# Optimization experiments

Hardware: AMD Instinct MI355X
Metric: run time of the kernel (lower is better)

## Reference

```python
import jax, jax.numpy as jnp
import numpy as np

LOG2E = 1.4426950408889634  # 1/ln(2): convert natural-log gates to log2 space (kernel uses exp2)
BT = 64  # chunk size


def setup_inputs() -> dict:
    key = jax.random.key(0)
    ks = jax.random.split(key, 5)
    B, H, T, K, V = 4, 8, 4096, 128, 128
    return {
        "q": jax.random.normal(ks[0], (B, H, T, K), dtype=jnp.float32),
        "k": jax.random.normal(ks[1], (B, H, T, K), dtype=jnp.float32),
        "v": jax.random.normal(ks[2], (B, H, T, V), dtype=jnp.float32),
        "i_gate": jax.random.normal(ks[3], (B, H, T), dtype=jnp.float32),
        "f_gate": jax.random.normal(ks[4], (B, H, T), dtype=jnp.float32),
    }


def reference(q, k, v, i_gate, f_gate):
    B, H, T, K = q.shape
    V = v.shape[-1]
    NT = T // BT
    scale = K ** -0.5

    # gate preprocessing: log-sigmoid forget gate, both gates moved to log2 space
    vecF = jax.nn.log_sigmoid(f_gate) * LOG2E  # [B,H,T]
    vecI = i_gate * LOG2E                      # [B,H,T]

    f_c = vecF.reshape(B, H, NT, BT)
    i_c = vecI.reshape(B, H, NT, BT)
    qc = q.reshape(B, H, NT, BT, K)
    kc = k.reshape(B, H, NT, BT, K)
    vc = v.reshape(B, H, NT, BT, V)

    vecB = jnp.cumsum(f_c, axis=-1)            # inclusive cumsum of f within chunk [B,H,NT,BT]
    scaG = vecB[..., -1]                       # total decay per chunk [B,H,NT]
    vecA = i_c + (scaG[..., None] - vecB)      # i_j + sum of f after j within chunk

    # ---- inter-chunk recurrence over matrix state C, normalizer n, max m ----
    kx = jnp.moveaxis(kc, 2, 0)  # [NT,B,H,BT,K]
    vx = jnp.moveaxis(vc, 2, 0)
    ax = jnp.moveaxis(vecA, 2, 0)  # [NT,B,H,BT]
    gx = jnp.moveaxis(scaG, 2, 0)  # [NT,B,H]

    C0 = jnp.zeros((B, H, K, V), dtype=q.dtype)
    n0 = jnp.zeros((B, H, K), dtype=q.dtype)
    m0 = jnp.zeros((B, H), dtype=q.dtype)

    def step(carry, inp):
        C, n, m = carry
        kk, vv, a, g = inp
        m_next = jnp.maximum(g + m, jnp.max(a, axis=-1))      # running stabilizer max
        dec = jnp.exp2(g + m - m_next)                        # [B,H]
        kbar = kk * jnp.exp2(a - m_next[..., None])[..., None]
        C_next = C * dec[..., None, None] + jnp.einsum('bhtk,bhtv->bhkv', kbar, vv)
        n_next = n * dec[..., None] + kbar.sum(axis=-2)
        return (C_next, n_next, m_next), (C, n, m)

    _, (Cp, np_, mp) = jax.lax.scan(step, (C0, n0, m0), (kx, vx, ax, gx))
    Cp = jnp.moveaxis(Cp, 0, 2)   # state entering each chunk [B,H,NT,K,V]
    np_ = jnp.moveaxis(np_, 0, 2)  # [B,H,NT,K]
    mp = jnp.moveaxis(mp, 0, 2)   # [B,H,NT]

    # ---- intra-chunk parallel part ----
    idx = jnp.arange(BT)
    causal = idx[:, None] >= idx[None, :]  # query i attends key j<=i
    # logD[i,j] = B_i - B_j + I_j for j<=i
    logD = vecB[..., :, None] - vecB[..., None, :] + i_c[..., None, :]
    logD = jnp.where(causal, logD, -jnp.inf)
    m_intra = logD.max(axis=-1)                                   # [B,H,NT,BT]
    m_comb = jnp.maximum(mp[..., None] + vecB, m_intra)           # total stabilizer per row
    D = jnp.exp2(logD - m_comb[..., None])                        # masked entries -> 0

    S = jnp.einsum('bhcik,bhcjk->bhcij', qc, kc) * scale * D
    qbar = qc * (scale * jnp.exp2(vecB + mp[..., None] - m_comb))[..., None]

    Hnum = jnp.einsum('bhcik,bhckv->bhciv', qbar, Cp) + jnp.einsum('bhcij,bhcjv->bhciv', S, vc)
    den = jnp.einsum('bhcik,bhck->bhci', qbar, np_) + S.sum(axis=-1)
    norm = jnp.maximum(jnp.abs(den), jnp.exp2(-m_comb))
    h = Hnum / norm[..., None]
    return h.reshape(B, H, T, V)
```

## Files before the change

### kernel.cpp

```cpp
#include <hip/hip_runtime.h>
#include <hip/hip_bf16.h>
#include <math.h>


#define LOG2E 1.4426950408889634f
constexpr int Bsz = 4, Hsz = 8, Tsz = 4096, Ksz = 128, Vsz = 128;
constexpr int BT = 64, NT = 64, BH = Bsz * Hsz;
constexpr float SCALE = 0.08838834764831845f;

typedef __attribute__((ext_vector_type(8))) short short8v;
typedef __attribute__((ext_vector_type(4))) float f32x4;
typedef __attribute__((ext_vector_type(4))) unsigned short u16x4;
typedef __attribute__((ext_vector_type(8))) unsigned short u16x8;

__device__ inline float bf2f(unsigned short u) {
    union { unsigned int i; float f; } c; c.i = ((unsigned int)u) << 16; return c.f;
}
__device__ inline unsigned short f2bf(float f) {
    __hip_bfloat16 h = __float2bfloat16(f);
    union { __hip_bfloat16 b; unsigned short u; } cv; cv.b = h; return cv.u;
}

__global__ __launch_bounds__(64) void k_gates(
    const float* __restrict__ ig, const float* __restrict__ fg,
    float* __restrict__ vecB, float* __restrict__ vecI, float* __restrict__ vecA,
    float* __restrict__ mintra, float* __restrict__ scaG, float* __restrict__ scaA)
{
    int c = blockIdx.x, bh = blockIdx.y, lane = threadIdx.x;
    int t = bh * Tsz + c * BT + lane;
    float f = fg[t];
    float ls = fminf(f, 0.f) - log1pf(expf(-fabsf(f)));
    float vF = ls * LOG2E;
    float vI = ig[t] * LOG2E;
    float b = vF;
    #pragma unroll
    for (int off = 1; off < 64; off <<= 1) {
        float o = __shfl_up(b, off, 64);
        if (lane >= off) b += o;
    }
    float g = __shfl(b, 63, 64);
    float mi = vI - b;
    #pragma unroll
    for (int off = 1; off < 64; off <<= 1) {
        float o = __shfl_up(mi, off, 64);
        if (lane >= off) mi = fmaxf(mi, o);
    }
    float a = vI + g - b;
    vecB[t] = b; vecI[t] = vI; vecA[t] = a; mintra[t] = b + mi;
    float am = a;
    #pragma unroll
    for (int off = 32; off; off >>= 1) am = fmaxf(am, __shfl_xor(am, off, 64));
    if (lane == 0) { scaG[bh * NT + c] = g; scaA[bh * NT + c] = am; }
}

__global__ __launch_bounds__(64) void k_mscan(
    const float* __restrict__ scaG, const float* __restrict__ scaA,
    float* __restrict__ mp, float* __restrict__ dec)
{
    int bh = blockIdx.x, lane = threadIdx.x;
    float g0 = scaG[bh * NT + lane];
    float a = g0, b = scaA[bh * NT + lane];
    #pragma unroll
    for (int off = 1; off < 64; off <<= 1) {
        float ap = __shfl_up(a, off, 64);
        float bp = __shfl_up(b, off, 64);
        if (lane >= off) { b = fmaxf(bp + a, b); a = ap + a; }
    }
    float m_incl = fmaxf(a, b);
    float m_prev = __shfl_up(m_incl, 1, 64);
    if (lane == 0) { m_prev = 0.f; mp[bh * (NT + 1)] = 0.f; }
    mp[bh * (NT + 1) + lane + 1] = m_incl;
    dec[bh * NT + lane] = exp2f(g0 + m_prev - m_incl);
}

__global__ __launch_bounds__(256, 4) void k_state(
    const float* __restrict__ kg, const float* __restrict__ vg,
    const float* __restrict__ vecA, const float* __restrict__ mp,
    unsigned short* __restrict__ UT, float* __restrict__ nU)
{
    int c = blockIdx.x, bh = blockIdx.y, tid = threadIdx.x;
    int lane = tid & 63, wid = tid >> 6;
    int lrow = lane & 15, kgrp = lane >> 4;

    __shared__ __align__(16) unsigned short kThi[128][72];
    __shared__ __align__(16) unsigned short vTs[128][72];
    __shared__ float nUp[128][5];

    size_t hb = (size_t)bh * Tsz + (size_t)c * BT;
    float mpn = mp[bh * (NT + 1) + c + 1];

    int cb = tid & 15, jr = tid >> 4;
    int wboff = (((jr >> 1) ^ (cb & 7)) * 16) + (jr & 1) * 8;
    float s4[4];
    #pragma unroll
    for (int x = 0; x < 4; ++x) s4[x] = exp2f(vecA[hb + jr * 4 + x] - mpn);
    #pragma unroll
    for (int p = 0; p < 2; ++p) {
        int c0 = p * 64 + cb * 4;
        float ka[4][4], va[4][4];
        #pragma unroll
        for (int x = 0; x < 4; ++x) {
            float4 kr = *(const float4*)(kg + (hb + jr * 4 + x) * Ksz + c0);
            float4 vr = *(const float4*)(vg + (hb + jr * 4 + x) * Vsz + c0);
            ka[x][0] = kr.x; ka[x][1] = kr.y; ka[x][2] = kr.z; ka[x][3] = kr.w;
            va[x][0] = vr.x; va[x][1] = vr.y; va[x][2] = vr.z; va[x][3] = vr.w;
        }
        #pragma unroll
        for (int y = 0; y < 4; ++y) {
            u16x4 h, w;
            float psum = 0.f;
            #pragma unroll
            for (int x = 0; x < 4; ++x) {
                float f = ka[x][y] * s4[x];
                h[x] = f2bf(f);
                psum += f;
                w[x] = f2bf(va[x][y]);
            }
            *(u16x4*)((char*)&kThi[c0 + y][0] + wboff) = h;
            *(u16x4*)((char*)&vTs[c0 + y][0] + wboff) = w;
            psum += __shfl_xor(psum, 16, 64);
            psum += __shfl_xor(psum, 32, 64);
            if (kgrp == 0) nUp[c0 + y][wid] = psum;
        }
    }
    __syncthreads();

    f32x4 acc[2][8];
    #pragma unroll
    for (int kt = 0; kt < 2; ++kt)
        #pragma unroll
        for (int vt = 0; vt < 8; ++vt) acc[kt][vt] = (f32x4){0.f, 0.f, 0.f, 0.f};
    #pragma unroll
    for (int ks = 0; ks < 2; ++ks) {
        int G = ks * 4 + kgrp;
        #pragma unroll
        for (int kt = 0; kt < 2; ++kt) {
            int arow = (wid * 2 + kt) * 16 + lrow;
            short8v af = *(const short8v*)((const char*)&kThi[arow][0]
                                           + ((G ^ ((arow >> 2) & 7)) * 16));
            #pragma unroll
            for (int vt = 0; vt < 8; ++vt) {
                int brow = vt * 16 + lrow;
                short8v bv = *(const short8v*)((const char*)&vTs[brow][0]
                                               + ((G ^ ((brow >> 2) & 7)) * 16));
                acc[kt][vt] = __builtin_amdgcn_mfma_f32_16x16x32_bf16(af, bv, acc[kt][vt], 0, 0, 0);
            }
        }
    }
    unsigned short* Ub = UT + (size_t)(bh * NT + c) * (Ksz * Vsz);
    #pragma unroll
    for (int kt = 0; kt < 2; ++kt) {
        int ktile = wid * 2 + kt;
        #pragma unroll
        for (int vt = 0; vt < 8; ++vt) {
            u16x4 w;
            #pragma unroll
            for (int r = 0; r < 4; ++r) w[r] = f2bf(acc[kt][vt][r]);
            *(u16x4*)(Ub + ((size_t)(ktile * 8 + vt) * 64 + lane) * 4) = w;
        }
    }
    if (tid < Ksz) {
        float s = nUp[tid][0] + nUp[tid][1] + nUp[tid][2] + nUp[tid][3];
        nU[(size_t)(bh * NT + c) * Ksz + tid] = s;
    }
}

__global__ __launch_bounds__(128) void k_scan(
    unsigned short* __restrict__ UT, const float* __restrict__ dec,
    const float* __restrict__ nU, float* __restrict__ np)
{
    int s = blockIdx.x, bh = blockIdx.y, tid = threadIdx.x;
    __shared__ float decs[NT];
    if (tid < NT) decs[tid] = dec[bh * NT + tid];
    __syncthreads();
    if (s == 32) {
        float n = 0.f;
        size_t base = (size_t)bh * NT * Ksz + tid;
        #pragma unroll 4
        for (int c2 = 0; c2 < NT; ++c2) {
            float u = nU[base + (size_t)c2 * Ksz];
            np[base + (size_t)c2 * Ksz] = n;
            n = n * decs[c2] + u;
        }
        return;
    }
    size_t base = (size_t)bh * NT * (Ksz * Vsz) + s * 512 + tid * 4;
    float C0 = 0.f, C1 = 0.f, C2 = 0.f, C3 = 0.f;
    #pragma unroll 4
    for (int c2 = 0; c2 < NT; ++c2) {
        size_t idx = base + (size_t)c2 * (Ksz * Vsz);
        u16x4 u = *(const u16x4*)(UT + idx);
        u16x4 w;
        w.x = f2bf(C0); w.y = f2bf(C1); w.z = f2bf(C2); w.w = f2bf(C3);
        *(u16x4*)(UT + idx) = w;
        float d = decs[c2];
        C0 = C0 * d + bf2f(u.x); C1 = C1 * d + bf2f(u.y);
        C2 = C2 * d + bf2f(u.z); C3 = C3 * d + bf2f(u.w);
    }
}

__global__ __launch_bounds__(256, 4) void k_intra(
    const float* __restrict__ qg, const float* __restrict__ kgl, const float* __restrict__ vg,
    const float* __restrict__ vecB, const float* __restrict__ vecI,
    const float* __restrict__ mintra, const float* __restrict__ mp,
    const float* __restrict__ np, const unsigned short* __restrict__ CpT,
    float* __restrict__ out)
{
    int c = blockIdx.x, bh = blockIdx.y, tid = threadIdx.x;
    int lane = tid & 63, wid = tid >> 6;
    int lrow = lane & 15, kgrp = lane >> 4;

    __shared__ __align__(16) unsigned short R[17408];
    __shared__ float rowf[BT], colf[BT], sfqs[BT], emcs[BT], denb[BT], npv[Ksz];

    auto khi = (unsigned short(*)[136])R;
    auto klo = (unsigned short(*)[136])(R + 64 * 136);
    auto Sb  = (unsigned short(*)[72])R;
    unsigned short* vTf = R + 64 * 72;
    unsigned short* cpsF = R;

    size_t hb = (size_t)bh * Tsz + (size_t)c * BT;
    float mpc = mp[bh * (NT + 1) + c];
    if (tid < BT) {
        float b = vecB[hb + tid];
        float mc = fmaxf(mpc + b, mintra[hb + tid]);
        rowf[tid] = SCALE * exp2f(b - mc);
        colf[tid] = exp2f(vecI[hb + tid] - b);
        sfqs[tid] = SCALE * exp2f(b + mpc - mc);
        emcs[tid] = exp2f(-mc);
    }
    if (tid < Ksz) npv[tid] = np[((size_t)bh * NT + c) * Ksz + tid];

    const float4* k4 = (const float4*)(kgl + hb * Ksz);
    for (int e = tid; e < BT * Ksz / 4; e += 256) {
        int i = e >> 5, c4 = (e & 31) * 4;
        float4 kv = k4[e];
        u16x4 h, l;
        h.x = f2bf(kv.x); l.x = f2bf(kv.x - bf2f(h.x));
        h.y = f2bf(kv.y); l.y = f2bf(kv.y - bf2f(h.y));
        h.z = f2bf(kv.z); l.z = f2bf(kv.z - bf2f(h.z));
        h.w = f2bf(kv.w); l.w = f2bf(kv.w - bf2f(h.w));
        *(u16x4*)&khi[i][c4] = h; *(u16x4*)&klo[i][c4] = l;
    }
    const float* qrow = qg + (hb + wid * 16 + lrow) * Ksz;
    float qf[4][8];
    #pragma unroll
    for (int ks = 0; ks < 4; ++ks) {
        float4 a = *(const float4*)(qrow + ks * 32 + kgrp * 8);
        float4 b = *(const float4*)(qrow + ks * 32 + kgrp * 8 + 4);
        qf[ks][0] = a.x; qf[ks][1] = a.y; qf[ks][2] = a.z; qf[ks][3] = a.w;
        qf[ks][4] = b.x; qf[ks][5] = b.y; qf[ks][6] = b.z; qf[ks][7] = b.w;
    }
    int vcb = tid & 15, jb = tid >> 4;
    float vpre[2][4][4];
    #pragma unroll
    for (int p = 0; p < 2; ++p)
        #pragma unroll
        for (int x = 0; x < 4; ++x) {
            float4 r4 = *(const float4*)(vg + (hb + jb * 4 + x) * Vsz + p * 64 + vcb * 4);
            vpre[p][x][0] = r4.x; vpre[p][x][1] = r4.y; vpre[p][x][2] = r4.z; vpre[p][x][3] = r4.w;
        }
    __syncthreads();

    float dot = 0.f;
    #pragma unroll
    for (int ks = 0; ks < 4; ++ks)
        #pragma unroll
        for (int x = 0; x < 8; ++x) dot += qf[ks][x] * npv[ks * 32 + kgrp * 8 + x];
    dot += __shfl_xor(dot, 16, 64);
    dot += __shfl_xor(dot, 32, 64);
    float qdot = sfqs[wid * 16 + lrow] * dot;

    short8v qh[4], ql[4];
    #pragma unroll
    for (int ks = 0; ks < 4; ++ks)
        #pragma unroll
        for (int x = 0; x < 8; ++x) {
            float f = qf[ks][x];
            unsigned short hh = f2bf(f);
            qh[ks][x] = (short)hh;
            ql[ks][x] = (short)f2bf(f - bf2f(hh));
        }

    f32x4 accS[4];
    #pragma unroll
    for (int jt = 0; jt < 4; ++jt) accS[jt] = (f32x4){0.f, 0.f, 0.f, 0.f};
    #pragma unroll
    for (int ks = 0; ks < 4; ++ks) {
        #pragma unroll
        for (int jt = 0; jt < 4; ++jt) {
            if (jt <= wid) {
                short8v bh_ = *(const short8v*)&khi[jt * 16 + lrow][ks * 32 + kgrp * 8];
                short8v bl  = *(const short8v*)&klo[jt * 16 + lrow][ks * 32 + kgrp * 8];
                accS[jt] = __builtin_amdgcn_mfma_f32_16x16x32_bf16(qh[ks], bh_, accS[jt], 0, 0, 0);
                accS[jt] = __builtin_amdgcn_mfma_f32_16x16x32_bf16(ql[ks], bh_, accS[jt], 0, 0, 0);
                accS[jt] = __builtin_amdgcn_mfma_f32_16x16x32_bf16(qh[ks], bl,  accS[jt], 0, 0, 0);
            }
        }
    }

    float rsum[4] = {0.f, 0.f, 0.f, 0.f};
    unsigned short sreg[4][4];
    #pragma unroll
    for (int jt = 0; jt < 4; ++jt)
        #pragma unroll
        for (int r = 0; r < 4; ++r) {
            int i = wid * 16 + kgrp * 4 + r, j = jt * 16 + lrow;
            float val = (j <= i) ? accS[jt][r] * rowf[i] * colf[j] : 0.f;
            rsum[r] += val;
            sreg[jt][r] = f2bf(val);
        }
    #pragma unroll
    for (int r = 0; r < 4; ++r) {
        rsum[r] += __shfl_xor(rsum[r], 1, 64);
        rsum[r] += __shfl_xor(rsum[r], 2, 64);
        rsum[r] += __shfl_xor(rsum[r], 4, 64);
        rsum[r] += __shfl_xor(rsum[r], 8, 64);
    }
    float qd[4];
    #pragma unroll
    for (int r = 0; r < 4; ++r) qd[r] = __shfl(qdot, kgrp * 4 + r, 64);
    if (lrow == 0) {
        #pragma unroll
        for (int r = 0; r < 4; ++r) {
            int i = wid * 16 + kgrp * 4 + r;
            float den = qd[r] + rsum[r];
            denb[i] = 1.f / fmaxf(fabsf(den), emcs[i]);
        }
    }
    __syncthreads();

    const u16x8* Cg = (const u16x8*)(CpT + ((size_t)bh * NT + c) * (Ksz * Vsz));
    u16x8 cpre[8];
    #pragma unroll
    for (int p2 = 0; p2 < 8; ++p2) cpre[p2] = Cg[tid + p2 * 256];

    #pragma unroll
    for (int jt = 0; jt < 4; ++jt)
        #pragma unroll
        for (int r = 0; r < 4; ++r)
            Sb[wid * 16 + kgrp * 4 + r][jt * 16 + lrow] = sreg[jt][r];
    #pragma unroll
    for (int p = 0; p < 2; ++p)
        #pragma unroll
        for (int y = 0; y < 4; ++y) {
            int row = p * 64 + vcb * 4 + y;
            int swzb = (jb * 8) ^ ((row & 7) << 4);
            u16x4 w;
            #pragma unroll
            for (int x = 0; x < 4; ++x) w[x] = f2bf(vpre[p][x][y]);
            *(u16x4*)((char*)(vTf + row * 64) + swzb) = w;
        }
    __syncthreads();

    f32x4 accV[8];
    #pragma unroll
    for (int vt = 0; vt < 8; ++vt) accV[vt] = (f32x4){0.f, 0.f, 0.f, 0.f};
    #pragma unroll
    for (int ks = 0; ks < 2; ++ks) {
        short8v as_ = *(const short8v*)&Sb[wid * 16 + lrow][ks * 32 + kgrp * 8];
        #pragma unroll
        for (int vt = 0; vt < 8; ++vt) {
            int row = vt * 16 + lrow;
            int swzb = ((ks * 64 + kgrp * 16)) ^ ((row & 7) << 4);
            short8v bv = *(const short8v*)((const char*)(vTf + row * 64) + swzb);
            accV[vt] = __builtin_amdgcn_mfma_f32_16x16x32_bf16(as_, bv, accV[vt], 0, 0, 0);
        }
    }
    __syncthreads();

    #pragma unroll
    for (int p2 = 0; p2 < 8; ++p2) {
        int idx = tid + p2 * 256;
        *(u16x8*)&cpsF[idx * 8] = cpre[p2];
    }
    __syncthreads();

    f32x4 accC[8];
    #pragma unroll
    for (int vt = 0; vt < 8; ++vt) accC[vt] = (f32x4){0.f, 0.f, 0.f, 0.f};
    #pragma unroll
    for (int ks = 0; ks < 4; ++ks) {
        int ktile = ks * 2 + (kgrp >> 1);
        int lsrc = (kgrp & 1) * 32 + lrow;
        #pragma unroll
        for (int vt = 0; vt < 8; ++vt) {
            const unsigned short* pf = &cpsF[((ktile * 8 + vt) * 64 + lsrc) * 4];
            u16x4 lo4 = *(const u16x4*)pf;
            u16x4 hi4 = *(const u16x4*)(pf + 64);
            short8v bc;
            bc[0] = (short)lo4.x; bc[1] = (short)lo4.y; bc[2] = (short)lo4.z; bc[3] = (short)lo4.w;
            bc[4] = (short)hi4.x; bc[5] = (short)hi4.y; bc[6] = (short)hi4.z; bc[7] = (short)hi4.w;
            accC[vt] = __builtin_amdgcn_mfma_f32_16x16x32_bf16(qh[ks], bc, accC[vt], 0, 0, 0);
            accC[vt] = __builtin_amdgcn_mfma_f32_16x16x32_bf16(ql[ks], bc, accC[vt], 0, 0, 0);
        }
    }
    size_t gb = hb * Vsz;
    #pragma unroll
    for (int vt = 0; vt < 8; ++vt)
        #pragma unroll
        for (int r = 0; r < 4; ++r) {
            int i = wid * 16 + kgrp * 4 + r, vc = vt * 16 + lrow;
            out[gb + (size_t)i * Vsz + vc] = (sfqs[i] * accC[vt][r] + accV[vt][r]) * denb[i];
        }
}

extern "C" void kernel_launch(void* const* d_in, const int* in_sizes, int n_in,
                              void* d_out, int out_size, void* d_ws, size_t ws_size,
                              hipStream_t stream) {
    const float* q  = (const float*)d_in[0];
    const float* k  = (const float*)d_in[1];
    const float* v  = (const float*)d_in[2];
    const float* ig = (const float*)d_in[3];
    const float* fg = (const float*)d_in[4];
    float* out = (float*)d_out;

    float* ws = (float*)d_ws;
    float* vecB   = ws;
    float* vecI   = vecB + BH * Tsz;
    float* vecA   = vecI + BH * Tsz;
    float* mintra = vecA + BH * Tsz;
    float* scaG   = mintra + BH * Tsz;
    float* scaA   = scaG + BH * NT;
    float* dec    = scaA + BH * NT;
    float* mp     = dec + BH * NT;
    float* nU     = mp + BH * (NT + 1);
    float* np     = nU + BH * NT * Ksz;
    unsigned short* UT = (unsigned short*)(np + BH * NT * Ksz);

    k_gates<<<dim3(NT, BH), 64, 0, stream>>>(ig, fg, vecB, vecI, vecA, mintra, scaG, scaA);
    k_mscan<<<dim3(BH), 64, 0, stream>>>(scaG, scaA, mp, dec);
    k_state<<<dim3(NT, BH), 256, 0, stream>>>(k, v, vecA, mp, UT, nU);
    k_scan<<<dim3(33, BH), 128, 0, stream>>>(UT, dec, nU, np);
    k_intra<<<dim3(NT, BH), 256, 0, stream>>>(q, k, v, vecB, vecI, mintra, mp, np, UT, out);
}
```

Baseline: 119.7 us.

## Process four chunks per k_state block with double-buffered LDS and prefetch

k_state now handles CPB=4 chunks per block. It double-buffers the transposed k/v tiles in LDS and issues global loads for the next chunk into registers while the MFMA accumulation of the current chunk runs. The aim is to hide global load latency behind compute and to amortise block setup. The cost is more registers for the prefetch buffers, a launch bound lowered to 2 waves per SIMD, double the LDS, and a grid reduced to 512 blocks, which may lower occupancy and parallelism.

```diff
diff --git a/kernel.cpp b/kernel.cpp
--- a/kernel.cpp
+++ b/kernel.cpp
@@ -7,6 +7,7 @@
 constexpr int Bsz = 4, Hsz = 8, Tsz = 4096, Ksz = 128, Vsz = 128;
 constexpr int BT = 64, NT = 64, BH = Bsz * Hsz;
 constexpr float SCALE = 0.08838834764831845f;
+constexpr int CPB = 4;
 
 typedef __attribute__((ext_vector_type(8))) short short8v;
 typedef __attribute__((ext_vector_type(4))) float f32x4;
@@ -19,6 +20,9 @@
 __device__ inline unsigned short f2bf(float f) {
     __hip_bfloat16 h = __float2bfloat16(f);
     union { __hip_bfloat16 b; unsigned short u; } cv; cv.b = h; return cv.u;
+}
+__device__ inline float f4c(const float4& v, int y) {
+    return y == 0 ? v.x : y == 1 ? v.y : y == 2 ? v.z : v.w;
 }
 
 __global__ __launch_bounds__(64) void k_gates(
@@ -73,95 +77,116 @@
     dec[bh * NT + lane] = exp2f(g0 + m_prev - m_incl);
 }
 
-__global__ __launch_bounds__(256, 4) void k_state(
+__global__ __launch_bounds__(256, 2) void k_state(
     const float* __restrict__ kg, const float* __restrict__ vg,
     const float* __restrict__ vecA, const float* __restrict__ mp,
     unsigned short* __restrict__ UT, float* __restrict__ nU)
 {
-    int c = blockIdx.x, bh = blockIdx.y, tid = threadIdx.x;
+    int c0 = blockIdx.x * CPB, bh = blockIdx.y, tid = threadIdx.x;
     int lane = tid & 63, wid = tid >> 6;
     int lrow = lane & 15, kgrp = lane >> 4;
 
-    __shared__ __align__(16) unsigned short kThi[128][72];
-    __shared__ __align__(16) unsigned short vTs[128][72];
-    __shared__ float nUp[128][5];
-
-    size_t hb = (size_t)bh * Tsz + (size_t)c * BT;
-    float mpn = mp[bh * (NT + 1) + c + 1];
+    __shared__ __align__(16) unsigned short kT[2][128][72];
+    __shared__ __align__(16) unsigned short vT[2][128][72];
+    __shared__ float nUp[2][128][5];
 
     int cb = tid & 15, jr = tid >> 4;
     int wboff = (((jr >> 1) ^ (cb & 7)) * 16) + (jr & 1) * 8;
-    float s4[4];
-    #pragma unroll
-    for (int x = 0; x < 4; ++x) s4[x] = exp2f(vecA[hb + jr * 4 + x] - mpn);
-    #pragma unroll
-    for (int p = 0; p < 2; ++p) {
-        int c0 = p * 64 + cb * 4;
-        float ka[4][4], va[4][4];
-        #pragma unroll
-        for (int x = 0; x < 4; ++x) {
-            float4 kr = *(const float4*)(kg + (hb + jr * 4 + x) * Ksz + c0);
-            float4 vr = *(const float4*)(vg + (hb + jr * 4 + x) * Vsz + c0);
-            ka[x][0] = kr.x; ka[x][1] = kr.y; ka[x][2] = kr.z; ka[x][3] = kr.w;
-            va[x][0] = vr.x; va[x][1] = vr.y; va[x][2] = vr.z; va[x][3] = vr.w;
-        }
-        #pragma unroll
-        for (int y = 0; y < 4; ++y) {
-            u16x4 h, w;
-            float psum = 0.f;
-            #pragma unroll
-            for (int x = 0; x < 4; ++x) {
-                float f = ka[x][y] * s4[x];
-                h[x] = f2bf(f);
-                psum += f;
-                w[x] = f2bf(va[x][y]);
+    const float* mpb = mp + bh * (NT + 1);
+
+    float4 kreg[4][2], vreg[4][2];
+
+    auto issue_loads = [&](int cc) {
+        size_t hbc = (size_t)bh * Tsz + (size_t)(c0 + cc) * BT;
+        #pragma unroll
+        for (int x = 0; x < 4; ++x)
+            #pragma unroll
+            for (int p = 0; p < 2; ++p) {
+                kreg[x][p] = *(const float4*)(kg + (hbc + jr * 4 + x) * Ksz + p * 64 + cb * 4);
+                vreg[x][p] = *(const float4*)(vg + (hbc + jr * 4 + x) * Vsz + p * 64 + cb * 4);
             }
-            *(u16x4*)((char*)&kThi[c0 + y][0] + wboff) = h;
-            *(u16x4*)((char*)&vTs[c0 + y][0] + wboff) = w;
-            psum += __shfl_xor(psum, 16, 64);
-            psum += __shfl_xor(psum, 32, 64);
-            if (kgrp == 0) nUp[c0 + y][wid] = psum;
-        }
-    }
-    __syncthreads();
-
-    f32x4 acc[2][8];
-    #pragma unroll
-    for (int kt = 0; kt < 2; ++kt)
-        #pragma unroll
-        for (int vt = 0; vt < 8; ++vt) acc[kt][vt] = (f32x4){0.f, 0.f, 0.f, 0.f};
-    #pragma unroll
-    for (int ks = 0; ks < 2; ++ks) {
-        int G = ks * 4 + kgrp;
+    };
+    auto cvt_store = [&](int cc, int b) {
+        size_t hbc = (size_t)bh * Tsz + (size_t)(c0 + cc) * BT;
+        float mpn = mpb[c0 + cc + 1];
+        float s4[4];
+        #pragma unroll
+        for (int x = 0; x < 4; ++x) s4[x] = exp2f(vecA[hbc + jr * 4 + x] - mpn);
+        #pragma unroll
+        for (int p = 0; p < 2; ++p) {
+            int cb0 = p * 64 + cb * 4;
+            #pragma unroll
+            for (int y = 0; y < 4; ++y) {
+                u16x4 h, w;
+                float psum = 0.f;
+                #pragma unroll
+                for (int x = 0; x < 4; ++x) {
+                    float kf = f4c(kreg[x][p], y) * s4[x];
+                    h[x] = f2bf(kf);
+                    psum += kf;
+                    w[x] = f2bf(f4c(vreg[x][p], y));
+                }
+                *(u16x4*)((char*)&kT[b][cb0 + y][0] + wboff) = h;
+                *(u16x4*)((char*)&vT[b][cb0 + y][0] + wboff) = w;
+                psum += __shfl_xor(psum, 16, 64);
+                psum += __shfl_xor(psum, 32, 64);
+                if (kgrp == 0) nUp[b][cb0 + y][wid] = psum;
+            }
+        }
+    };
+
+    issue_loads(0);
+    cvt_store(0, 0);
+    __syncthreads();
+
+    int b = 0;
+    for (int cc = 0; cc < CPB; ++cc) {
+        if (cc + 1 < CPB) issue_loads(cc + 1);
+
+        f32x4 acc[2][8];
+        #pragma unroll
+        for (int kt = 0; kt < 2; ++kt)
+            #pragma unroll
+            for (int vt = 0; vt < 8; ++vt) acc[kt][vt] = (f32x4){0.f, 0.f, 0.f, 0.f};
+        #pragma unroll
+        for (int ks = 0; ks < 2; ++ks) {
+            int G = ks * 4 + kgrp;
+            #pragma unroll
+            for (int kt = 0; kt < 2; ++kt) {
+                int arow = (wid * 2 + kt) * 16 + lrow;
+                short8v af = *(const short8v*)((const char*)&kT[b][arow][0]
+                                               + ((G ^ ((arow >> 2) & 7)) * 16));
+                #pragma unroll
+                for (int vt = 0; vt < 8; ++vt) {
+                    int brow = vt * 16 + lrow;
+                    short8v bv = *(const short8v*)((const char*)&vT[b][brow][0]
+                                                   + ((G ^ ((brow >> 2) & 7)) * 16));
+                    acc[kt][vt] = __builtin_amdgcn_mfma_f32_16x16x32_bf16(af, bv, acc[kt][vt], 0, 0, 0);
+                }
+            }
+        }
+        unsigned short* Ub = UT + (size_t)(bh * NT + c0 + cc) * (Ksz * Vsz);
         #pragma unroll
         for (int kt = 0; kt < 2; ++kt) {
-            int arow = (wid * 2 + kt) * 16 + lrow;
-            short8v af = *(const short8v*)((const char*)&kThi[arow][0]
-                                           + ((G ^ ((arow >> 2) & 7)) * 16));
+            int ktile = wid * 2 + kt;
             #pragma unroll
             for (int vt = 0; vt < 8; ++vt) {
-                int brow = vt * 16 + lrow;
-                short8v bv = *(const short8v*)((const char*)&vTs[brow][0]
-                                               + ((G ^ ((brow >> 2) & 7)) * 16));
-                acc[kt][vt] = __builtin_amdgcn_mfma_f32_16x16x32_bf16(af, bv, acc[kt][vt], 0, 0, 0);
+                u16x4 w;
+                #pragma unroll
+                for (int r = 0; r < 4; ++r) w[r] = f2bf(acc[kt][vt][r]);
+                *(u16x4*)(Ub + ((size_t)(ktile * 8 + vt) * 64 + lane) * 4) = w;
             }
         }
-    }
-    unsigned short* Ub = UT + (size_t)(bh * NT + c) * (Ksz * Vsz);
-    #pragma unroll
-    for (int kt = 0; kt < 2; ++kt) {
-        int ktile = wid * 2 + kt;
-        #pragma unroll
-        for (int vt = 0; vt < 8; ++vt) {
-            u16x4 w;
-            #pragma unroll
-            for (int r = 0; r < 4; ++r) w[r] = f2bf(acc[kt][vt][r]);
-            *(u16x4*)(Ub + ((size_t)(ktile * 8 + vt) * 64 + lane) * 4) = w;
-        }
-    }
-    if (tid < Ksz) {
-        float s = nUp[tid][0] + nUp[tid][1] + nUp[tid][2] + nUp[tid][3];
-        nU[(size_t)(bh * NT + c) * Ksz + tid] = s;
+        if (tid < Ksz) {
+            float s = nUp[b][tid][0] + nUp[b][tid][1] + nUp[b][tid][2] + nUp[b][tid][3];
+            nU[(size_t)(bh * NT + c0 + cc) * Ksz + tid] = s;
+        }
+
+        if (cc + 1 < CPB) {
+            cvt_store(cc + 1, b ^ 1);
+            __syncthreads();
+            b ^= 1;
+        }
     }
 }
 
@@ -430,7 +455,7 @@
 
     k_gates<<<dim3(NT, BH), 64, 0, stream>>>(ig, fg, vecB, vecI, vecA, mintra, scaG, scaA);
     k_mscan<<<dim3(BH), 64, 0, stream>>>(scaG, scaA, mp, dec);
-    k_state<<<dim3(NT, BH), 256, 0, stream>>>(k, v, vecA, mp, UT, nU);
+    k_state<<<dim3(NT / CPB, BH), 256, 0, stream>>>(k, v, vecA, mp, UT, nU);
     k_scan<<<dim3(33, BH), 128, 0, stream>>>(UT, dec, nU, np);
     k_intra<<<dim3(NT, BH), 256, 0, stream>>>(q, k, v, vecB, vecI, mintra, mp, np, UT, out);
 }
```

Measured after the change: 124.9 us. 4.3% more time.
